# Kernel optimization log

Hardware: AMD Instinct MI355X
Metric: run time of the kernel (lower is better)

Reference implementation:

```python
import jax, jax.numpy as jnp
import numpy as np

NEG_SLOPE = 0.2  # PyG GATConv default negative_slope


def _gat_edge_forward(x, edge_index, edge_attr, W, W_edge, att_src, att_dst, att_edge, bias):
    N = x.shape[0]
    H, C = att_src.shape
    src, dst = edge_index[0], edge_index[1]

    # --- add self loops with edge_attr fill_value='mean' (PyG default) ---
    ones = jnp.ones((edge_attr.shape[0],), dtype=x.dtype)
    cnt = jax.ops.segment_sum(ones, dst, num_segments=N)  # [N]
    attr_sum = jax.ops.segment_sum(edge_attr, dst, num_segments=N)  # [N, edge_dim]
    loop_attr = attr_sum / jnp.maximum(cnt, 1.0)[:, None]  # mean, 0 if no in-edges
    loop_idx = jnp.arange(N, dtype=edge_index.dtype)
    src_all = jnp.concatenate([src, loop_idx])
    dst_all = jnp.concatenate([dst, loop_idx])
    attr_all = jnp.concatenate([edge_attr, loop_attr], axis=0)  # [E+N, edge_dim]

    # --- linear projections ---
    x_l = (x @ W).reshape(N, H, C)  # [N,H,C]; GATConv uses same lin for src/dst
    a_src = jnp.einsum('nhc,hc->nh', x_l, att_src)  # [N,H]
    a_dst = jnp.einsum('nhc,hc->nh', x_l, att_dst)  # [N,H]
    e = (attr_all @ W_edge).reshape(-1, H, C)  # [E+N,H,C]
    a_edge = jnp.einsum('ehc,hc->eh', e, att_edge)  # [E+N,H]

    # --- per-edge attention logits + segment softmax over incoming edges ---
    logits = jax.nn.leaky_relu(a_src[src_all] + a_dst[dst_all] + a_edge, NEG_SLOPE)
    m = jax.ops.segment_max(logits, dst_all, num_segments=N)  # [N,H]
    p = jnp.exp(logits - m[dst_all])
    denom = jax.ops.segment_sum(p, dst_all, num_segments=N)  # [N,H]
    alpha = p / denom[dst_all]  # [E+N,H]

    # --- weighted scatter aggregation ---
    msgs = alpha[:, :, None] * x_l[src_all]  # [E+N,H,C]
    out = jax.ops.segment_sum(msgs, dst_all, num_segments=N)  # [N,H,C]
    return out.reshape(N, H * C) + bias  # concat=True -> [N, H*C]


def setup_inputs() -> dict:
    key = jax.random.key(0)
    ks = jax.random.split(key, 8)
    N, E, DIN, EDIM, H, C = 100000, 1600000, 128, 16, 4, 32
    s = 1.0 / np.sqrt(DIN)
    return {
        'x': jax.random.normal(ks[0], (N, DIN), jnp.float32),
        'edge_index': jax.random.randint(ks[1], (2, E), 0, N, jnp.int64),
        'edge_attr': jax.random.normal(ks[2], (E, EDIM), jnp.float32),
        'W': jax.random.normal(ks[3], (DIN, H * C), jnp.float32) * s,
        'W_edge': jax.random.normal(ks[4], (EDIM, H * C), jnp.float32) * (1.0 / np.sqrt(EDIM)),
        'att_src': jax.random.normal(ks[5], (H, C), jnp.float32) * 0.1,
        'att_dst': jax.random.normal(ks[6], (H, C), jnp.float32) * 0.1,
        'att_edge': jax.random.normal(ks[7], (H, C), jnp.float32) * 0.1,
        'bias': jnp.zeros((H * C,), jnp.float32),
    }


def reference(x, edge_index, edge_attr, W, W_edge, att_src, att_dst, att_edge, bias):
    return _gat_edge_forward(x, edge_index, edge_attr, W, W_edge, att_src, att_dst, att_edge, bias)
```

## Files before the change

kernel.cpp:

```cpp
#include <hip/hip_runtime.h>
#include <hip/hip_fp16.h>
#include <math.h>

#define NEG_SLOPE 0.2f
typedef unsigned short ushort_t;
typedef unsigned int uint_t;

__global__ void k0_vedge(const float* __restrict__ W_edge, const float* __restrict__ att_edge,
                         float* __restrict__ v_edge) {
  int t = threadIdx.x;
  int h = t >> 4, j = t & 15;
  float s = 0.f;
#pragma unroll
  for (int c = 0; c < 32; ++c) s += W_edge[j * 128 + h * 32 + c] * att_edge[h * 32 + c];
  v_edge[t] = s;
}

__global__ void k_detect(const int* __restrict__ ei, int* __restrict__ flag) {
  __shared__ int any;
  if (threadIdx.x == 0) any = 0;
  __syncthreads();
  if (ei[2 * threadIdx.x + 1] != 0) atomicOr(&any, 1);
  __syncthreads();
  if (threadIdx.x == 0) *flag = (any == 0) ? 1 : 0;
}

__global__ void k_zero(int* __restrict__ p, int n) {
  int i = blockIdx.x * blockDim.x + threadIdx.x;
  if (i < n) p[i] = 0;
}

__global__ __launch_bounds__(256) void k1_xl(
    const float* __restrict__ x, const float* __restrict__ W,
    const float* __restrict__ att_src, const float* __restrict__ att_dst,
    ushort_t* __restrict__ x_l_h, float* __restrict__ a_src, float* __restrict__ a_dst, int N) {
  __shared__ float Wc[32 * 128];
  __shared__ float Xc[32 * 64];
  const int t = threadIdx.x;
  const int tcol = t & 31;
  const int trow = t >> 5;
  const int row0 = blockIdx.x * 64;
  const int r = t & 63, kq = t >> 6;
  const float4 aw_s = *(const float4*)&att_src[tcol * 4];
  const float4 aw_d = *(const float4*)&att_dst[tcol * 4];
  float acc[8][4];
#pragma unroll
  for (int i = 0; i < 8; ++i) { acc[i][0] = acc[i][1] = acc[i][2] = acc[i][3] = 0.f; }

  for (int kc = 0; kc < 4; ++kc) {
    float4 wreg[4];
#pragma unroll
    for (int q = 0; q < 4; ++q) wreg[q] = *(const float4*)&W[kc * 4096 + (q * 256 + t) * 4];
    float xs8[8];
    int grow = row0 + r;
    if (grow < N) {
      *(float4*)&xs8[0] = *(const float4*)&x[grow * 128 + kc * 32 + kq * 8];
      *(float4*)&xs8[4] = *(const float4*)&x[grow * 128 + kc * 32 + kq * 8 + 4];
    } else {
#pragma unroll
      for (int q = 0; q < 8; ++q) xs8[q] = 0.f;
    }
    __syncthreads();
#pragma unroll
    for (int q = 0; q < 4; ++q) *(float4*)&Wc[(q * 256 + t) * 4] = wreg[q];
#pragma unroll
    for (int q = 0; q < 8; ++q) Xc[(kq * 8 + q) * 64 + r] = xs8[q];
    __syncthreads();
#pragma unroll
    for (int kk = 0; kk < 32; ++kk) {
      float4 wv = *(const float4*)&Wc[kk * 128 + tcol * 4];
      float xr[8];
      *(float4*)&xr[0] = *(const float4*)&Xc[kk * 64 + trow * 8];
      *(float4*)&xr[4] = *(const float4*)&Xc[kk * 64 + trow * 8 + 4];
#pragma unroll
      for (int ri = 0; ri < 8; ++ri) {
        acc[ri][0] += xr[ri] * wv.x;
        acc[ri][1] += xr[ri] * wv.y;
        acc[ri][2] += xr[ri] * wv.z;
        acc[ri][3] += xr[ri] * wv.w;
      }
    }
  }
#pragma unroll
  for (int ri = 0; ri < 8; ++ri) {
    int grow = row0 + trow * 8 + ri;
    float asp = acc[ri][0] * aw_s.x + acc[ri][1] * aw_s.y + acc[ri][2] * aw_s.z + acc[ri][3] * aw_s.w;
    float adp = acc[ri][0] * aw_d.x + acc[ri][1] * aw_d.y + acc[ri][2] * aw_d.z + acc[ri][3] * aw_d.w;
#pragma unroll
    for (int m = 1; m < 8; m <<= 1) { asp += __shfl_xor(asp, m); adp += __shfl_xor(adp, m); }
    if (grow < N) {
      __half2 h0 = __floats2half2_rn(acc[ri][0], acc[ri][1]);
      __half2 h1 = __floats2half2_rn(acc[ri][2], acc[ri][3]);
      uint2 u; u.x = *(uint_t*)&h0; u.y = *(uint_t*)&h1;
      *(uint2*)&x_l_h[(size_t)grow * 128 + tcol * 4] = u;
      if ((tcol & 7) == 0) {
        a_src[grow * 4 + (tcol >> 3)] = asp;
        a_dst[grow * 4 + (tcol >> 3)] = adp;
      }
    }
  }
}

__global__ void k_hist(const int* __restrict__ ei, const int* __restrict__ is64,
                       int* __restrict__ deg, int E) {
  int i = blockIdx.x * blockDim.x + threadIdx.x;
  if (i >= E) return;
  int dst = (*is64) ? ei[2 * (E + i)] : ei[E + i];
  atomicAdd(&deg[dst], 1);
}

__global__ void k_scan1(const int* __restrict__ deg, int* __restrict__ bsum, int N) {
  __shared__ int lds[256];
  int b = blockIdx.x, t = threadIdx.x;
  int base = b * 1024 + t * 4;
  int s = 0;
  if (base + 3 < N) {
    int4 v = *(const int4*)&deg[base];
    s = v.x + v.y + v.z + v.w;
  } else {
    for (int q = 0; q < 4; ++q) if (base + q < N) s += deg[base + q];
  }
  lds[t] = s; __syncthreads();
  for (int st = 128; st > 0; st >>= 1) {
    if (t < st) lds[t] += lds[t + st];
    __syncthreads();
  }
  if (t == 0) bsum[b] = lds[0];
}

__global__ void k_scan2(const int* __restrict__ bsum, int* __restrict__ boff, int NB) {
  __shared__ int lds[256];
  int t = threadIdx.x;
  int v = (t < NB) ? bsum[t] : 0;
  lds[t] = v;
  __syncthreads();
  for (int st = 1; st < 256; st <<= 1) {
    int add = (t >= st) ? lds[t - st] : 0;
    __syncthreads();
    lds[t] += add;
    __syncthreads();
  }
  if (t < NB) boff[t] = lds[t] - v;
}

__global__ void k_scan3(const int* __restrict__ deg, const int* __restrict__ boff,
                        int* __restrict__ offs, int* __restrict__ cursor, int N) {
  __shared__ int lds[256];
  int b = blockIdx.x, t = threadIdx.x;
  int base = b * 1024 + t * 4;
  int v[4]; int s = 0;
#pragma unroll
  for (int q = 0; q < 4; ++q) { v[q] = (base + q < N) ? deg[base + q] : 0; s += v[q]; }
  lds[t] = s;
  __syncthreads();
  for (int st = 1; st < 256; st <<= 1) {
    int add = (t >= st) ? lds[t - st] : 0;
    __syncthreads();
    lds[t] += add;
    __syncthreads();
  }
  int run = boff[b] + lds[t] - s;
#pragma unroll
  for (int q = 0; q < 4; ++q) {
    if (base + q < N) { offs[base + q] = run; cursor[base + q] = run; }
    run += v[q];
  }
}

__global__ __launch_bounds__(256) void k_scatter(
    const int* __restrict__ ei, const int* __restrict__ is64,
    const float* __restrict__ edge_attr, const float* __restrict__ v_edge,
    int* __restrict__ cursor, float* __restrict__ rec, int E) {
  __shared__ float ve[64];
  int t = threadIdx.x;
  if (t < 64) ve[t] = v_edge[t];
  __syncthreads();
  int i = blockIdx.x * 256 + t;
  if (i >= E) return;
  int f = *is64;
  int src = f ? ei[2 * i] : ei[i];
  int dst = f ? ei[2 * (E + i)] : ei[E + i];
  float a16[16];
  *(float4*)&a16[0]  = *(const float4*)&edge_attr[(size_t)i * 16];
  *(float4*)&a16[4]  = *(const float4*)&edge_attr[(size_t)i * 16 + 4];
  *(float4*)&a16[8]  = *(const float4*)&edge_attr[(size_t)i * 16 + 8];
  *(float4*)&a16[12] = *(const float4*)&edge_attr[(size_t)i * 16 + 12];
  float ae[4];
#pragma unroll
  for (int h = 0; h < 4; ++h) {
    float s = 0.f;
#pragma unroll
    for (int j = 0; j < 16; ++j) s += a16[j] * ve[h * 16 + j];
    ae[h] = s;
  }
  int pos = atomicAdd(&cursor[dst], 1);
  float4 r0; r0.x = ae[0]; r0.y = ae[1]; r0.z = ae[2]; r0.w = ae[3];
  float4 r1; r1.x = __int_as_float(src); r1.y = 0.f; r1.z = 0.f; r1.w = 0.f;
  *(float4*)&rec[(size_t)pos * 8]     = r0;
  *(float4*)&rec[(size_t)pos * 8 + 4] = r1;
}

__global__ __launch_bounds__(256) void k3_softmax(
    float* __restrict__ rec, const float* __restrict__ a_src,
    const float* __restrict__ a_dst, const int* __restrict__ deg,
    const int* __restrict__ offs, float* __restrict__ inv_den,
    float* __restrict__ aloop, int N) {
  int t = threadIdx.x;
  int node = blockIdx.x * 16 + (t >> 4);
  int sl = t & 15;
  if (node >= N) return;
  int off = offs[node], dg = deg[node];
  float ad4[4]; *(float4*)ad4 = *(const float4*)&a_dst[(size_t)node * 4];
  const int* reci = (const int*)rec;
  float den[4] = {0, 0, 0, 0}, sae[4] = {0, 0, 0, 0};
  for (int i = sl; i < dg; i += 16) {
    size_t p = (size_t)(off + i) * 8;
    float aev[4]; *(float4*)aev = *(const float4*)&rec[p];
    int src = reci[p + 4];
    float as4[4]; *(float4*)as4 = *(const float4*)&a_src[(size_t)src * 4];
    float p4[4];
#pragma unroll
    for (int h = 0; h < 4; ++h) {
      float lg = as4[h] + ad4[h] + aev[h];
      lg = (lg >= 0.f) ? lg : NEG_SLOPE * lg;
      float pv = __expf(lg);
      p4[h] = pv;
      den[h] += pv;
      sae[h] += aev[h];
    }
    *(float4*)&rec[p] = *(float4*)p4;
  }
#pragma unroll
  for (int m = 1; m < 16; m <<= 1) {
#pragma unroll
    for (int h = 0; h < 4; ++h) { den[h] += __shfl_xor(den[h], m); sae[h] += __shfl_xor(sae[h], m); }
  }
  if (sl == 0) {
    float as4[4]; *(float4*)as4 = *(const float4*)&a_src[(size_t)node * 4];
    float inv_cnt = 1.f / (float)(dg > 0 ? dg : 1);
    float id4[4], al4[4];
#pragma unroll
    for (int h = 0; h < 4; ++h) {
      float lae = sae[h] * inv_cnt;
      float lg = as4[h] + ad4[h] + lae;
      lg = (lg >= 0.f) ? lg : NEG_SLOPE * lg;
      float pl = __expf(lg);
      float dt = den[h] + pl;
      float iv = 1.f / dt;
      id4[h] = iv; al4[h] = pl * iv;
    }
    *(float4*)&inv_den[(size_t)node * 4] = *(float4*)id4;
    *(float4*)&aloop[(size_t)node * 4]  = *(float4*)al4;
  }
}

__global__ __launch_bounds__(256) void k4_agg(
    const float* __restrict__ rec, const ushort_t* __restrict__ x_l_h,
    const float* __restrict__ inv_den, const float* __restrict__ aloop,
    const int* __restrict__ deg, const int* __restrict__ offs,
    const float* __restrict__ bias, float* __restrict__ out, int N) {
  int lane = threadIdx.x & 63;
  int node = blockIdx.x * 4 + (threadIdx.x >> 6);
  if (node >= N) return;
  int off = offs[node], dg = deg[node];
  int h = lane >> 4;
  float iv = inv_den[(size_t)node * 4 + h];
  float al = aloop[(size_t)node * 4 + h];
  const uint_t* xu = (const uint_t*)x_l_h;
  const int* reci = (const int*)rec;
  float accx, accy;
  {
    uint_t v = xu[(size_t)node * 64 + lane];
    float2 f = __half22float2(*(const __half2*)&v);
    accx = al * f.x; accy = al * f.y;
  }
  int i = 0;
  for (; i + 4 <= dg; i += 4) {
    size_t p0 = (size_t)(off + i) * 8, p1 = p0 + 8, p2 = p0 + 16, p3 = p0 + 24;
    float a0 = rec[p0 + h], a1 = rec[p1 + h], a2 = rec[p2 + h], a3 = rec[p3 + h];
    int s0 = reci[p0 + 4], s1 = reci[p1 + 4], s2 = reci[p2 + 4], s3 = reci[p3 + 4];
    uint_t v0 = xu[(size_t)s0 * 64 + lane];
    uint_t v1 = xu[(size_t)s1 * 64 + lane];
    uint_t v2 = xu[(size_t)s2 * 64 + lane];
    uint_t v3 = xu[(size_t)s3 * 64 + lane];
    float2 f0 = __half22float2(*(const __half2*)&v0);
    float2 f1 = __half22float2(*(const __half2*)&v1);
    float2 f2 = __half22float2(*(const __half2*)&v2);
    float2 f3 = __half22float2(*(const __half2*)&v3);
    a0 *= iv; a1 *= iv; a2 *= iv; a3 *= iv;
    accx += a0 * f0.x; accy += a0 * f0.y;
    accx += a1 * f1.x; accy += a1 * f1.y;
    accx += a2 * f2.x; accy += a2 * f2.y;
    accx += a3 * f3.x; accy += a3 * f3.y;
  }
  for (; i < dg; ++i) {
    size_t p = (size_t)(off + i) * 8;
    float a = rec[p + h] * iv;
    int s = reci[p + 4];
    uint_t v = xu[(size_t)s * 64 + lane];
    float2 f = __half22float2(*(const __half2*)&v);
    accx += a * f.x; accy += a * f.y;
  }
  float2 b2 = *(const float2*)&bias[2 * lane];
  float2 o; o.x = accx + b2.x; o.y = accy + b2.y;
  *(float2*)&out[(size_t)node * 128 + 2 * lane] = o;
}

extern "C" void kernel_launch(void* const* d_in, const int* in_sizes, int n_in,
                              void* d_out, int out_size, void* d_ws, size_t ws_size,
                              hipStream_t stream) {
  const float* x        = (const float*)d_in[0];
  const int*   ei       = (const int*)  d_in[1];
  const float* eattr    = (const float*)d_in[2];
  const float* W        = (const float*)d_in[3];
  const float* W_edge   = (const float*)d_in[4];
  const float* att_src  = (const float*)d_in[5];
  const float* att_dst  = (const float*)d_in[6];
  const float* att_edge = (const float*)d_in[7];
  const float* bias     = (const float*)d_in[8];
  float* out = (float*)d_out;
  const int N = in_sizes[0] / 128;
  const int E = in_sizes[1] / 2;
  (void)n_in; (void)out_size; (void)ws_size;

  char* base = (char*)d_ws;
  size_t off = 0;
  auto take = [&](size_t bytes) -> void* {
    void* p = base + off;
    off = (off + bytes + 255) & ~(size_t)255;
    return p;
  };
  ushort_t* x_l_h  = (ushort_t*)take((size_t)N * 128 * 2);
  float* a_src    = (float*)take((size_t)N * 4 * 4);
  float* a_dst    = (float*)take((size_t)N * 4 * 4);
  float* v_edge   = (float*)take(64 * 4);
  float* rec      = (float*)take((size_t)E * 32);
  float* inv_den  = (float*)take((size_t)N * 4 * 4);
  float* aloop    = (float*)take((size_t)N * 4 * 4);
  int*   deg      = (int*)take((size_t)N * 4);
  int*   offs     = (int*)take((size_t)N * 4);
  int*   cursor   = (int*)take((size_t)N * 4);
  int*   bsum     = (int*)take(256 * 4);
  int*   boff     = (int*)take(256 * 4);
  int*   is64     = (int*)take(4);

  const int NB = (N + 1023) / 1024;

  hipLaunchKernelGGL(k_detect, dim3(1), dim3(256), 0, stream, ei, is64);
  hipLaunchKernelGGL(k_zero, dim3((N + 255) / 256), dim3(256), 0, stream, deg, N);
  hipLaunchKernelGGL(k0_vedge, dim3(1), dim3(64), 0, stream, W_edge, att_edge, v_edge);
  hipLaunchKernelGGL(k1_xl, dim3((N + 63) / 64), dim3(256), 0, stream,
                     x, W, att_src, att_dst, x_l_h, a_src, a_dst, N);
  hipLaunchKernelGGL(k_hist, dim3((E + 255) / 256), dim3(256), 0, stream, ei, is64, deg, E);
  hipLaunchKernelGGL(k_scan1, dim3(NB), dim3(256), 0, stream, deg, bsum, N);
  hipLaunchKernelGGL(k_scan2, dim3(1), dim3(256), 0, stream, bsum, boff, NB);
  hipLaunchKernelGGL(k_scan3, dim3(NB), dim3(256), 0, stream, deg, boff, offs, cursor, N);
  hipLaunchKernelGGL(k_scatter, dim3((E + 255) / 256), dim3(256), 0, stream,
                     ei, is64, eattr, v_edge, cursor, rec, E);
  hipLaunchKernelGGL(k3_softmax, dim3((N + 15) / 16), dim3(256), 0, stream,
                     rec, a_src, a_dst, deg, offs, inv_den, aloop, N);
  hipLaunchKernelGGL(k4_agg, dim3((N + 3) / 4), dim3(256), 0, stream,
                     rec, x_l_h, inv_den, aloop, deg, offs, bias, out, N);
}
```

Measured before the change: 333.2 us.

## Pack edge records to fp16 and replace scatter atomics with precomputed ranks

Edge records shrink from 32 to 16 bytes by storing the edge logits and softmax numerators as fp16, with the source index in the same int4. The degree histogram now records each edge's rank, so the scatter computes its slot as offset plus rank instead of a second atomic pass, and the cursor array is dropped. Three small setup kernels are merged into one launch. This cuts memory traffic and atomic contention, at the cost of an extra per-edge rank array and reduced precision (and possible overflow) in the stored exp values.

Result: faster. 300.7 us (-9.8%).

```diff
diff --git a/kernel.cpp b/kernel.cpp
--- a/kernel.cpp
+++ b/kernel.cpp
@@ -6,28 +6,30 @@
 typedef unsigned short ushort_t;
 typedef unsigned int uint_t;
 
-__global__ void k0_vedge(const float* __restrict__ W_edge, const float* __restrict__ att_edge,
-                         float* __restrict__ v_edge) {
-  int t = threadIdx.x;
-  int h = t >> 4, j = t & 15;
-  float s = 0.f;
-#pragma unroll
-  for (int c = 0; c < 32; ++c) s += W_edge[j * 128 + h * 32 + c] * att_edge[h * 32 + c];
-  v_edge[t] = s;
-}
-
-__global__ void k_detect(const int* __restrict__ ei, int* __restrict__ flag) {
-  __shared__ int any;
-  if (threadIdx.x == 0) any = 0;
-  __syncthreads();
-  if (ei[2 * threadIdx.x + 1] != 0) atomicOr(&any, 1);
-  __syncthreads();
-  if (threadIdx.x == 0) *flag = (any == 0) ? 1 : 0;
-}
-
-__global__ void k_zero(int* __restrict__ p, int n) {
-  int i = blockIdx.x * blockDim.x + threadIdx.x;
-  if (i < n) p[i] = 0;
+__global__ void k_prep(const int* __restrict__ ei, int* __restrict__ is64,
+                       int* __restrict__ deg, int N,
+                       const float* __restrict__ W_edge, const float* __restrict__ att_edge,
+                       float* __restrict__ v_edge) {
+  int b = blockIdx.x, t = threadIdx.x;
+  if (b == 0) {
+    __shared__ int any;
+    if (t == 0) any = 0;
+    __syncthreads();
+    if (ei[2 * t + 1] != 0) atomicOr(&any, 1);
+    __syncthreads();
+    if (t == 0) *is64 = (any == 0) ? 1 : 0;
+  } else if (b == 1) {
+    if (t < 64) {
+      int h = t >> 4, j = t & 15;
+      float s = 0.f;
+#pragma unroll
+      for (int c = 0; c < 32; ++c) s += W_edge[j * 128 + h * 32 + c] * att_edge[h * 32 + c];
+      v_edge[t] = s;
+    }
+  } else {
+    int i = (b - 2) * 256 + t;
+    if (i < N) deg[i] = 0;
+  }
 }
 
 __global__ __launch_bounds__(256) void k1_xl(
@@ -102,11 +104,11 @@
 }
 
 __global__ void k_hist(const int* __restrict__ ei, const int* __restrict__ is64,
-                       int* __restrict__ deg, int E) {
+                       int* __restrict__ deg, int* __restrict__ rank, int E) {
   int i = blockIdx.x * blockDim.x + threadIdx.x;
   if (i >= E) return;
   int dst = (*is64) ? ei[2 * (E + i)] : ei[E + i];
-  atomicAdd(&deg[dst], 1);
+  rank[i] = atomicAdd(&deg[dst], 1);
 }
 
 __global__ void k_scan1(const int* __restrict__ deg, int* __restrict__ bsum, int N) {
@@ -144,7 +146,7 @@
 }
 
 __global__ void k_scan3(const int* __restrict__ deg, const int* __restrict__ boff,
-                        int* __restrict__ offs, int* __restrict__ cursor, int N) {
+                        int* __restrict__ offs, int N) {
   __shared__ int lds[256];
   int b = blockIdx.x, t = threadIdx.x;
   int base = b * 1024 + t * 4;
@@ -162,15 +164,16 @@
   int run = boff[b] + lds[t] - s;
 #pragma unroll
   for (int q = 0; q < 4; ++q) {
-    if (base + q < N) { offs[base + q] = run; cursor[base + q] = run; }
+    if (base + q < N) offs[base + q] = run;
     run += v[q];
   }
 }
 
 __global__ __launch_bounds__(256) void k_scatter(
     const int* __restrict__ ei, const int* __restrict__ is64,
+    const int* __restrict__ rank, const int* __restrict__ offs,
     const float* __restrict__ edge_attr, const float* __restrict__ v_edge,
-    int* __restrict__ cursor, float* __restrict__ rec, int E) {
+    int4* __restrict__ rec, int E) {
   __shared__ float ve[64];
   int t = threadIdx.x;
   if (t < 64) ve[t] = v_edge[t];
@@ -193,15 +196,15 @@
     for (int j = 0; j < 16; ++j) s += a16[j] * ve[h * 16 + j];
     ae[h] = s;
   }
-  int pos = atomicAdd(&cursor[dst], 1);
-  float4 r0; r0.x = ae[0]; r0.y = ae[1]; r0.z = ae[2]; r0.w = ae[3];
-  float4 r1; r1.x = __int_as_float(src); r1.y = 0.f; r1.z = 0.f; r1.w = 0.f;
-  *(float4*)&rec[(size_t)pos * 8]     = r0;
-  *(float4*)&rec[(size_t)pos * 8 + 4] = r1;
+  int pos = offs[dst] + rank[i];
+  __half2 e01 = __floats2half2_rn(ae[0], ae[1]);
+  __half2 e23 = __floats2half2_rn(ae[2], ae[3]);
+  int4 r; r.x = *(int*)&e01; r.y = *(int*)&e23; r.z = src; r.w = 0;
+  rec[pos] = r;
 }
 
 __global__ __launch_bounds__(256) void k3_softmax(
-    float* __restrict__ rec, const float* __restrict__ a_src,
+    int4* __restrict__ rec, const float* __restrict__ a_src,
     const float* __restrict__ a_dst, const int* __restrict__ deg,
     const int* __restrict__ offs, float* __restrict__ inv_den,
     float* __restrict__ aloop, int N) {
@@ -211,12 +214,15 @@
   if (node >= N) return;
   int off = offs[node], dg = deg[node];
   float ad4[4]; *(float4*)ad4 = *(const float4*)&a_dst[(size_t)node * 4];
-  const int* reci = (const int*)rec;
+  uint2* rec8 = (uint2*)rec;
   float den[4] = {0, 0, 0, 0}, sae[4] = {0, 0, 0, 0};
   for (int i = sl; i < dg; i += 16) {
-    size_t p = (size_t)(off + i) * 8;
-    float aev[4]; *(float4*)aev = *(const float4*)&rec[p];
-    int src = reci[p + 4];
+    int pos = off + i;
+    int4 u = rec[pos];
+    float2 e01 = __half22float2(*(const __half2*)&u.x);
+    float2 e23 = __half22float2(*(const __half2*)&u.y);
+    float aev[4] = {e01.x, e01.y, e23.x, e23.y};
+    int src = u.z;
     float as4[4]; *(float4*)as4 = *(const float4*)&a_src[(size_t)src * 4];
     float p4[4];
 #pragma unroll
@@ -228,7 +234,10 @@
       den[h] += pv;
       sae[h] += aev[h];
     }
-    *(float4*)&rec[p] = *(float4*)p4;
+    __half2 p01 = __floats2half2_rn(p4[0], p4[1]);
+    __half2 p23 = __floats2half2_rn(p4[2], p4[3]);
+    uint2 w; w.x = *(uint_t*)&p01; w.y = *(uint_t*)&p23;
+    rec8[(size_t)pos * 2] = w;
   }
 #pragma unroll
   for (int m = 1; m < 16; m <<= 1) {
@@ -255,7 +264,7 @@
 }
 
 __global__ __launch_bounds__(256) void k4_agg(
-    const float* __restrict__ rec, const ushort_t* __restrict__ x_l_h,
+    const int4* __restrict__ rec, const ushort_t* __restrict__ x_l_h,
     const float* __restrict__ inv_den, const float* __restrict__ aloop,
     const int* __restrict__ deg, const int* __restrict__ offs,
     const float* __restrict__ bias, float* __restrict__ out, int N) {
@@ -267,7 +276,6 @@
   float iv = inv_den[(size_t)node * 4 + h];
   float al = aloop[(size_t)node * 4 + h];
   const uint_t* xu = (const uint_t*)x_l_h;
-  const int* reci = (const int*)rec;
   float accx, accy;
   {
     uint_t v = xu[(size_t)node * 64 + lane];
@@ -276,28 +284,38 @@
   }
   int i = 0;
   for (; i + 4 <= dg; i += 4) {
-    size_t p0 = (size_t)(off + i) * 8, p1 = p0 + 8, p2 = p0 + 16, p3 = p0 + 24;
-    float a0 = rec[p0 + h], a1 = rec[p1 + h], a2 = rec[p2 + h], a3 = rec[p3 + h];
-    int s0 = reci[p0 + 4], s1 = reci[p1 + 4], s2 = reci[p2 + 4], s3 = reci[p3 + 4];
-    uint_t v0 = xu[(size_t)s0 * 64 + lane];
-    uint_t v1 = xu[(size_t)s1 * 64 + lane];
-    uint_t v2 = xu[(size_t)s2 * 64 + lane];
-    uint_t v3 = xu[(size_t)s3 * 64 + lane];
+    int4 u0 = rec[off + i], u1 = rec[off + i + 1], u2 = rec[off + i + 2], u3 = rec[off + i + 3];
+    uint_t w0 = (h & 2) ? (uint_t)u0.y : (uint_t)u0.x;
+    uint_t w1 = (h & 2) ? (uint_t)u1.y : (uint_t)u1.x;
+    uint_t w2 = (h & 2) ? (uint_t)u2.y : (uint_t)u2.x;
+    uint_t w3 = (h & 2) ? (uint_t)u3.y : (uint_t)u3.x;
+    float2 q0 = __half22float2(*(const __half2*)&w0);
+    float2 q1 = __half22float2(*(const __half2*)&w1);
+    float2 q2 = __half22float2(*(const __half2*)&w2);
+    float2 q3 = __half22float2(*(const __half2*)&w3);
+    float a0 = ((h & 1) ? q0.y : q0.x) * iv;
+    float a1 = ((h & 1) ? q1.y : q1.x) * iv;
+    float a2 = ((h & 1) ? q2.y : q2.x) * iv;
+    float a3 = ((h & 1) ? q3.y : q3.x) * iv;
+    uint_t v0 = xu[(size_t)u0.z * 64 + lane];
+    uint_t v1 = xu[(size_t)u1.z * 64 + lane];
+    uint_t v2 = xu[(size_t)u2.z * 64 + lane];
+    uint_t v3 = xu[(size_t)u3.z * 64 + lane];
     float2 f0 = __half22float2(*(const __half2*)&v0);
     float2 f1 = __half22float2(*(const __half2*)&v1);
     float2 f2 = __half22float2(*(const __half2*)&v2);
     float2 f3 = __half22float2(*(const __half2*)&v3);
-    a0 *= iv; a1 *= iv; a2 *= iv; a3 *= iv;
     accx += a0 * f0.x; accy += a0 * f0.y;
     accx += a1 * f1.x; accy += a1 * f1.y;
     accx += a2 * f2.x; accy += a2 * f2.y;
     accx += a3 * f3.x; accy += a3 * f3.y;
   }
   for (; i < dg; ++i) {
-    size_t p = (size_t)(off + i) * 8;
-    float a = rec[p + h] * iv;
-    int s = reci[p + 4];
-    uint_t v = xu[(size_t)s * 64 + lane];
+    int4 u = rec[off + i];
+    uint_t w = (h & 2) ? (uint_t)u.y : (uint_t)u.x;
+    float2 q = __half22float2(*(const __half2*)&w);
+    float a = ((h & 1) ? q.y : q.x) * iv;
+    uint_t v = xu[(size_t)u.z * 64 + lane];
     float2 f = __half22float2(*(const __half2*)&v);
     accx += a * f.x; accy += a * f.y;
   }
@@ -330,33 +348,32 @@
     off = (off + bytes + 255) & ~(size_t)255;
     return p;
   };
-  ushort_t* x_l_h  = (ushort_t*)take((size_t)N * 128 * 2);
+  ushort_t* x_l_h = (ushort_t*)take((size_t)N * 128 * 2);
   float* a_src    = (float*)take((size_t)N * 4 * 4);
   float* a_dst    = (float*)take((size_t)N * 4 * 4);
   float* v_edge   = (float*)take(64 * 4);
-  float* rec      = (float*)take((size_t)E * 32);
+  int4*  rec      = (int4*)take((size_t)E * 16);
   float* inv_den  = (float*)take((size_t)N * 4 * 4);
   float* aloop    = (float*)take((size_t)N * 4 * 4);
   int*   deg      = (int*)take((size_t)N * 4);
   int*   offs     = (int*)take((size_t)N * 4);
-  int*   cursor   = (int*)take((size_t)N * 4);
+  int*   rank     = (int*)take((size_t)E * 4);
   int*   bsum     = (int*)take(256 * 4);
   int*   boff     = (int*)take(256 * 4);
   int*   is64     = (int*)take(4);
 
   const int NB = (N + 1023) / 1024;
 
-  hipLaunchKernelGGL(k_detect, dim3(1), dim3(256), 0, stream, ei, is64);
-  hipLaunchKernelGGL(k_zero, dim3((N + 255) / 256), dim3(256), 0, stream, deg, N);
-  hipLaunchKernelGGL(k0_vedge, dim3(1), dim3(64), 0, stream, W_edge, att_edge, v_edge);
+  hipLaunchKernelGGL(k_prep, dim3(2 + (N + 255) / 256), dim3(256), 0, stream,
+                     ei, is64, deg, N, W_edge, att_edge, v_edge);
   hipLaunchKernelGGL(k1_xl, dim3((N + 63) / 64), dim3(256), 0, stream,
                      x, W, att_src, att_dst, x_l_h, a_src, a_dst, N);
-  hipLaunchKernelGGL(k_hist, dim3((E + 255) / 256), dim3(256), 0, stream, ei, is64, deg, E);
+  hipLaunchKernelGGL(k_hist, dim3((E + 255) / 256), dim3(256), 0, stream, ei, is64, deg, rank, E);
   hipLaunchKernelGGL(k_scan1, dim3(NB), dim3(256), 0, stream, deg, bsum, N);
   hipLaunchKernelGGL(k_scan2, dim3(1), dim3(256), 0, stream, bsum, boff, NB);
-  hipLaunchKernelGGL(k_scan3, dim3(NB), dim3(256), 0, stream, deg, boff, offs, cursor, N);
+  hipLaunchKernelGGL(k_scan3, dim3(NB), dim3(256), 0, stream, deg, boff, offs, N);
   hipLaunchKernelGGL(k_scatter, dim3((E + 255) / 256), dim3(256), 0, stream,
-                     ei, is64, eattr, v_edge, cursor, rec, E);
+                     ei, is64, rank, offs, eattr, v_edge, rec, E);
   hipLaunchKernelGGL(k3_softmax, dim3((N + 15) / 16), dim3(256), 0, stream,
                      rec, a_src, a_dst, deg, offs, inv_den, aloop, N);
   hipLaunchKernelGGL(k4_agg, dim3((N + 3) / 4), dim3(256), 0, stream,
```
